# Performance work log

Hardware: AMD Instinct MI355X
Metric: run time of the kernel (lower is better)

The kernel has to match this reference:

```python
import jax, jax.numpy as jnp
import numpy as np


def setup_inputs() -> dict:
    key = jax.random.key(0)
    kq, kk, kv = jax.random.split(key, 3)
    B, N, M, H, D = 4, 2048, 2048, 8, 64
    queries = jax.random.normal(kq, (B, N, H, D), dtype=jnp.float32)
    keys = jax.random.normal(kk, (B, M, H, D), dtype=jnp.float32)
    values = jax.random.normal(kv, (B, M, H, D), dtype=jnp.float32)
    return {"queries": queries, "keys": keys, "values": values}


def reference(queries, keys, values):
    # queries: [B,N,H,D], keys/values: [B,M,H,D]
    D = queries.shape[3]
    softmax_temp = 1.0 / (D ** 0.5)
    QK = jnp.einsum('bnhd,bmhd->bnmh', queries, keys)  # [B,N,M,H]
    A = jax.nn.softmax(softmax_temp * QK, axis=2)      # softmax over M
    queried_values = jnp.einsum('bnmh,bmhd->bnhd', A, values)
    attention_weight = jnp.transpose(A, (0, 3, 1, 2))  # [B,H,N,M]
    return (queried_values, attention_weight)
```

## Files before the change

### kernel.cpp

```cpp
#include <hip/hip_runtime.h>

typedef __bf16 bf16x8 __attribute__((ext_vector_type(8)));
typedef float floatx4 __attribute__((ext_vector_type(4)));
typedef unsigned short ushort8 __attribute__((ext_vector_type(8)));
typedef unsigned short ushort4v __attribute__((ext_vector_type(4)));

#define MFMA(a, b, c) __builtin_amdgcn_mfma_f32_16x16x32_bf16((a), (b), (c), 0, 0, 0)

__device__ __forceinline__ unsigned short f2bf(float x) {
  union { float f; unsigned u; } v; v.f = x;
  unsigned r = v.u + 0x7FFFu + ((v.u >> 16) & 1u);
  return (unsigned short)(r >> 16);
}

constexpr int LD = 72;

__global__ __launch_bounds__(256, 4)
void attn_fwd(const float* __restrict__ Q, const float* __restrict__ K,
              const float* __restrict__ V, float* __restrict__ outQV,
              float* __restrict__ outA)
{
  __shared__ __align__(16) unsigned short Ks[64 * LD];
  __shared__ __align__(16) unsigned short Vts[64 * LD];
  __shared__ __align__(16) unsigned short As[64 * LD];

  const int tid = threadIdx.x;
  const int w  = tid >> 6;
  const int l  = tid & 63;
  const int c  = l & 15;
  const int q4 = l >> 4;

  const int bx = blockIdx.x;
  const int qt = bx & 31;
  const int h  = (bx >> 5) & 7;
  const int b  = bx >> 8;
  const int q0 = qt * 64;

  const float scale = 0.125f * 1.44269504088896340736f;

  const size_t base = (size_t)b * (2048 * 512) + (size_t)h * 64;
  const float* Qb = Q + base + (size_t)q0 * 512;
  const float* Kb = K + base;
  const float* Vb = V + base;

  const int r0 = tid >> 4;
  const int c4 = tid & 15;

  bf16x8 bQ0, bQ1;
  {
    const float* qp = Qb + (size_t)(16 * w + c) * 512 + q4 * 8;
    float4 qa0 = *(const float4*)(qp);
    float4 qa1 = *(const float4*)(qp + 4);
    float4 qb0 = *(const float4*)(qp + 32);
    float4 qb1 = *(const float4*)(qp + 36);
    ushort8 t0, t1;
    t0[0]=f2bf(qa0.x*scale); t0[1]=f2bf(qa0.y*scale); t0[2]=f2bf(qa0.z*scale); t0[3]=f2bf(qa0.w*scale);
    t0[4]=f2bf(qa1.x*scale); t0[5]=f2bf(qa1.y*scale); t0[6]=f2bf(qa1.z*scale); t0[7]=f2bf(qa1.w*scale);
    t1[0]=f2bf(qb0.x*scale); t1[1]=f2bf(qb0.y*scale); t1[2]=f2bf(qb0.z*scale); t1[3]=f2bf(qb0.w*scale);
    t1[4]=f2bf(qb1.x*scale); t1[5]=f2bf(qb1.y*scale); t1[6]=f2bf(qb1.z*scale); t1[7]=f2bf(qb1.w*scale);
    bQ0 = __builtin_bit_cast(bf16x8, t0);
    bQ1 = __builtin_bit_cast(bf16x8, t1);
  }

  float4 kreg[4];
  #pragma unroll
  for (int g = 0; g < 4; ++g)
    kreg[g] = *(const float4*)(Kb + (size_t)(r0 + 16 * g) * 512 + c4 * 4);

  float lsum[4] = {0.f, 0.f, 0.f, 0.f};
  for (int mc = 0; mc < 2048; mc += 64) {
    #pragma unroll
    for (int g = 0; g < 4; ++g) {
      unsigned short* dst = &Ks[(r0 + 16 * g) * LD + c4 * 4];
      dst[0] = f2bf(kreg[g].x); dst[1] = f2bf(kreg[g].y);
      dst[2] = f2bf(kreg[g].z); dst[3] = f2bf(kreg[g].w);
    }
    __syncthreads();
    if (mc + 64 < 2048) {
      #pragma unroll
      for (int g = 0; g < 4; ++g)
        kreg[g] = *(const float4*)(Kb + (size_t)(mc + 64 + r0 + 16 * g) * 512 + c4 * 4);
    }
    #pragma unroll
    for (int t = 0; t < 4; ++t) {
      bf16x8 aK0 = *(const bf16x8*)&Ks[(t * 16 + c) * LD + q4 * 8];
      bf16x8 aK1 = *(const bf16x8*)&Ks[(t * 16 + c) * LD + 32 + q4 * 8];
      floatx4 acc = {0.f, 0.f, 0.f, 0.f};
      acc = MFMA(aK0, bQ0, acc);
      acc = MFMA(aK1, bQ1, acc);
      #pragma unroll
      for (int i = 0; i < 4; ++i) lsum[i] += __builtin_amdgcn_exp2f(acc[i]);
    }
    __syncthreads();
  }
  float rs = (lsum[0] + lsum[1]) + (lsum[2] + lsum[3]);
  rs += __shfl_xor(rs, 16);
  rs += __shfl_xor(rs, 32);
  const float rcp = 1.0f / rs;

  floatx4 Oacc[4];
  #pragma unroll
  for (int t = 0; t < 4; ++t) Oacc[t] = (floatx4){0.f, 0.f, 0.f, 0.f};

  float* aRowP = outA + (((size_t)(b * 8 + h) * 2048 + q0 + 16 * w + c) * 2048) + q4 * 4;

  float4 vreg[4];
  #pragma unroll
  for (int g = 0; g < 4; ++g) {
    kreg[g] = *(const float4*)(Kb + (size_t)(r0 + 16 * g) * 512 + c4 * 4);
    vreg[g] = *(const float4*)(Vb + (size_t)(r0 + 16 * g) * 512 + c4 * 4);
  }

  for (int mc = 0; mc < 2048; mc += 64) {
    #pragma unroll
    for (int g = 0; g < 4; ++g) {
      unsigned short* dst = &Ks[(r0 + 16 * g) * LD + c4 * 4];
      dst[0] = f2bf(kreg[g].x); dst[1] = f2bf(kreg[g].y);
      dst[2] = f2bf(kreg[g].z); dst[3] = f2bf(kreg[g].w);
      int m = r0 + 16 * g;
      Vts[(c4 * 4 + 0) * LD + m] = f2bf(vreg[g].x);
      Vts[(c4 * 4 + 1) * LD + m] = f2bf(vreg[g].y);
      Vts[(c4 * 4 + 2) * LD + m] = f2bf(vreg[g].z);
      Vts[(c4 * 4 + 3) * LD + m] = f2bf(vreg[g].w);
    }
    __syncthreads();
    if (mc + 64 < 2048) {
      #pragma unroll
      for (int g = 0; g < 4; ++g) {
        kreg[g] = *(const float4*)(Kb + (size_t)(mc + 64 + r0 + 16 * g) * 512 + c4 * 4);
        vreg[g] = *(const float4*)(Vb + (size_t)(mc + 64 + r0 + 16 * g) * 512 + c4 * 4);
      }
    }
    #pragma unroll
    for (int t = 0; t < 4; ++t) {
      bf16x8 aK0 = *(const bf16x8*)&Ks[(t * 16 + c) * LD + q4 * 8];
      bf16x8 aK1 = *(const bf16x8*)&Ks[(t * 16 + c) * LD + 32 + q4 * 8];
      floatx4 acc = {0.f, 0.f, 0.f, 0.f};
      acc = MFMA(aK0, bQ0, acc);
      acc = MFMA(aK1, bQ1, acc);
      floatx4 av;
      av[0] = __builtin_amdgcn_exp2f(acc[0]) * rcp;
      av[1] = __builtin_amdgcn_exp2f(acc[1]) * rcp;
      av[2] = __builtin_amdgcn_exp2f(acc[2]) * rcp;
      av[3] = __builtin_amdgcn_exp2f(acc[3]) * rcp;
      __builtin_nontemporal_store(av, (floatx4*)(aRowP + mc + t * 16));
      ushort4v us = { f2bf(av[0]), f2bf(av[1]), f2bf(av[2]), f2bf(av[3]) };
      *(ushort4v*)&As[(16 * w + c) * LD + t * 16 + q4 * 4] = us;
    }
    bf16x8 aP0 = *(const bf16x8*)&As[(16 * w + c) * LD + q4 * 8];
    bf16x8 aP1 = *(const bf16x8*)&As[(16 * w + c) * LD + 32 + q4 * 8];
    #pragma unroll
    for (int t = 0; t < 4; ++t) {
      bf16x8 bV0 = *(const bf16x8*)&Vts[(t * 16 + c) * LD + q4 * 8];
      bf16x8 bV1 = *(const bf16x8*)&Vts[(t * 16 + c) * LD + 32 + q4 * 8];
      Oacc[t] = MFMA(aP0, bV0, Oacc[t]);
      Oacc[t] = MFMA(aP1, bV1, Oacc[t]);
    }
    __syncthreads();
  }

  #pragma unroll
  for (int t = 0; t < 4; ++t) {
    #pragma unroll
    for (int i = 0; i < 4; ++i) {
      outQV[base + (size_t)(q0 + 16 * w + q4 * 4 + i) * 512 + t * 16 + c] = Oacc[t][i];
    }
  }
}

extern "C" void kernel_launch(void* const* d_in, const int* in_sizes, int n_in,
                              void* d_out, int out_size, void* d_ws, size_t ws_size,
                              hipStream_t stream)
{
  const float* Q = (const float*)d_in[0];
  const float* K = (const float*)d_in[1];
  const float* V = (const float*)d_in[2];
  float* outQV = (float*)d_out;
  float* outA  = (float*)d_out + 4194304;
  attn_fwd<<<dim3(1024), dim3(256), 0, stream>>>(Q, K, V, outQV, outA);
}
```

Baseline: 723.0 us.

## Precompute bf16 K and transposed V, stream tiles via direct global-to-LDS double buffering

```diff
diff --git a/kernel.cpp b/kernel.cpp
--- a/kernel.cpp
+++ b/kernel.cpp
@@ -13,16 +13,61 @@
   return (unsigned short)(r >> 16);
 }
 
-constexpr int LD = 72;
+__global__ __launch_bounds__(256)
+void prep(const float* __restrict__ K, const float* __restrict__ V,
+          unsigned short* __restrict__ Kb, unsigned short* __restrict__ Vt)
+{
+  int id = blockIdx.x * 256 + threadIdx.x;
+  int isV = id >> 19;
+  int cch = id & 524287;
+  int bh = cch >> 14;
+  int mt = (cch >> 9) & 31;
+  int g  = cch & 511;
+  int r  = g >> 3;
+  int s  = g & 7;
+  int e8 = s ^ (r & 7);
+  int b = bh >> 3, h = bh & 7;
+  ushort8 o;
+  if (!isV) {
+    const float* p = K + (((size_t)(b * 2048 + mt * 64 + r) * 8 + h) * 64 + e8 * 8);
+    float4 x0 = *(const float4*)p;
+    float4 x1 = *(const float4*)(p + 4);
+    o[0] = f2bf(x0.x); o[1] = f2bf(x0.y); o[2] = f2bf(x0.z); o[3] = f2bf(x0.w);
+    o[4] = f2bf(x1.x); o[5] = f2bf(x1.y); o[6] = f2bf(x1.z); o[7] = f2bf(x1.w);
+    *(ushort8*)(Kb + (size_t)cch * 8) = o;
+  } else {
+    const float* p = V + (((size_t)(b * 2048 + mt * 64 + e8 * 8) * 8 + h) * 64 + r);
+    #pragma unroll
+    for (int j = 0; j < 8; ++j) o[j] = f2bf(p[(size_t)j * 512]);
+    *(ushort8*)(Vt + (size_t)cch * 8) = o;
+  }
+}
+
+__device__ __forceinline__ void stage2k(const unsigned short* gsrc, unsigned short* lds,
+                                        int w, int l)
+{
+  const char* g = (const char*)gsrc + w * 2048 + l * 16;
+  char* sd = (char*)lds + w * 2048;
+  __builtin_amdgcn_global_load_lds((const __attribute__((address_space(1))) unsigned int*)g,
+                                   (__attribute__((address_space(3))) unsigned int*)sd, 16, 0, 0);
+  __builtin_amdgcn_global_load_lds((const __attribute__((address_space(1))) unsigned int*)(g + 1024),
+                                   (__attribute__((address_space(3))) unsigned int*)(sd + 1024), 16, 0, 0);
+}
+
+__device__ __forceinline__ bf16x8 frag(const unsigned short* lds, int r, int bo)
+{
+  int slot = ((bo >> 4) ^ r) & 7;
+  return *(const bf16x8*)((const char*)lds + r * 128 + (slot << 4));
+}
 
 __global__ __launch_bounds__(256, 4)
-void attn_fwd(const float* __restrict__ Q, const float* __restrict__ K,
-              const float* __restrict__ V, float* __restrict__ outQV,
-              float* __restrict__ outA)
-{
-  __shared__ __align__(16) unsigned short Ks[64 * LD];
-  __shared__ __align__(16) unsigned short Vts[64 * LD];
-  __shared__ __align__(16) unsigned short As[64 * LD];
+void attn_fwd(const float* __restrict__ Q, const unsigned short* __restrict__ Kb,
+              const unsigned short* __restrict__ Vt,
+              float* __restrict__ outQV, float* __restrict__ outA)
+{
+  __shared__ __align__(16) unsigned short Ks[2][4096];
+  __shared__ __align__(16) unsigned short Vs[2][4096];
+  __shared__ __align__(16) unsigned short As[4096];
 
   const int tid = threadIdx.x;
   const int w  = tid >> 6;
@@ -40,11 +85,9 @@
 
   const size_t base = (size_t)b * (2048 * 512) + (size_t)h * 64;
   const float* Qb = Q + base + (size_t)q0 * 512;
-  const float* Kb = K + base;
-  const float* Vb = V + base;
-
-  const int r0 = tid >> 4;
-  const int c4 = tid & 15;
+
+  const unsigned short* Kt0 = Kb + (size_t)(b * 8 + h) * (32 * 4096);
+  const unsigned short* Vt0 = Vt + (size_t)(b * 8 + h) * (32 * 4096);
 
   bf16x8 bQ0, bQ1;
   {
@@ -62,36 +105,24 @@
     bQ1 = __builtin_bit_cast(bf16x8, t1);
   }
 
-  float4 kreg[4];
-  #pragma unroll
-  for (int g = 0; g < 4; ++g)
-    kreg[g] = *(const float4*)(Kb + (size_t)(r0 + 16 * g) * 512 + c4 * 4);
-
+  stage2k(Kt0, Ks[0], w, l);
   float lsum[4] = {0.f, 0.f, 0.f, 0.f};
-  for (int mc = 0; mc < 2048; mc += 64) {
-    #pragma unroll
-    for (int g = 0; g < 4; ++g) {
-      unsigned short* dst = &Ks[(r0 + 16 * g) * LD + c4 * 4];
-      dst[0] = f2bf(kreg[g].x); dst[1] = f2bf(kreg[g].y);
-      dst[2] = f2bf(kreg[g].z); dst[3] = f2bf(kreg[g].w);
-    }
+  int cur = 0;
+  for (int mt = 0; mt < 32; ++mt) {
     __syncthreads();
-    if (mc + 64 < 2048) {
-      #pragma unroll
-      for (int g = 0; g < 4; ++g)
-        kreg[g] = *(const float4*)(Kb + (size_t)(mc + 64 + r0 + 16 * g) * 512 + c4 * 4);
-    }
+    if (mt + 1 < 32) stage2k(Kt0 + (size_t)(mt + 1) * 4096, Ks[cur ^ 1], w, l);
+    const unsigned short* Kc = Ks[cur];
     #pragma unroll
     for (int t = 0; t < 4; ++t) {
-      bf16x8 aK0 = *(const bf16x8*)&Ks[(t * 16 + c) * LD + q4 * 8];
-      bf16x8 aK1 = *(const bf16x8*)&Ks[(t * 16 + c) * LD + 32 + q4 * 8];
+      bf16x8 aK0 = frag(Kc, t * 16 + c, q4 * 16);
+      bf16x8 aK1 = frag(Kc, t * 16 + c, 64 + q4 * 16);
       floatx4 acc = {0.f, 0.f, 0.f, 0.f};
       acc = MFMA(aK0, bQ0, acc);
       acc = MFMA(aK1, bQ1, acc);
       #pragma unroll
       for (int i = 0; i < 4; ++i) lsum[i] += __builtin_amdgcn_exp2f(acc[i]);
     }
-    __syncthreads();
+    cur ^= 1;
   }
   float rs = (lsum[0] + lsum[1]) + (lsum[2] + lsum[3]);
   rs += __shfl_xor(rs, 16);
@@ -102,39 +133,26 @@
   #pragma unroll
   for (int t = 0; t < 4; ++t) Oacc[t] = (floatx4){0.f, 0.f, 0.f, 0.f};
 
-  float* aRowP = outA + (((size_t)(b * 8 + h) * 2048 + q0 + 16 * w + c) * 2048) + q4 * 4;
-
-  float4 vreg[4];
-  #pragma unroll
-  for (int g = 0; g < 4; ++g) {
-    kreg[g] = *(const float4*)(Kb + (size_t)(r0 + 16 * g) * 512 + c4 * 4);
-    vreg[g] = *(const float4*)(Vb + (size_t)(r0 + 16 * g) * 512 + c4 * 4);
-  }
-
-  for (int mc = 0; mc < 2048; mc += 64) {
-    #pragma unroll
-    for (int g = 0; g < 4; ++g) {
-      unsigned short* dst = &Ks[(r0 + 16 * g) * LD + c4 * 4];
-      dst[0] = f2bf(kreg[g].x); dst[1] = f2bf(kreg[g].y);
-      dst[2] = f2bf(kreg[g].z); dst[3] = f2bf(kreg[g].w);
-      int m = r0 + 16 * g;
-      Vts[(c4 * 4 + 0) * LD + m] = f2bf(vreg[g].x);
-      Vts[(c4 * 4 + 1) * LD + m] = f2bf(vreg[g].y);
-      Vts[(c4 * 4 + 2) * LD + m] = f2bf(vreg[g].z);
-      Vts[(c4 * 4 + 3) * LD + m] = f2bf(vreg[g].w);
-    }
+  const int arow = 16 * w + c;
+  float* aRowP = outA + (((size_t)(b * 8 + h) * 2048 + q0 + arow) * 2048) + q4 * 4;
+
+  __syncthreads();
+  stage2k(Kt0, Ks[0], w, l);
+  stage2k(Vt0, Vs[0], w, l);
+  cur = 0;
+  for (int mt = 0; mt < 32; ++mt) {
     __syncthreads();
-    if (mc + 64 < 2048) {
-      #pragma unroll
-      for (int g = 0; g < 4; ++g) {
-        kreg[g] = *(const float4*)(Kb + (size_t)(mc + 64 + r0 + 16 * g) * 512 + c4 * 4);
-        vreg[g] = *(const float4*)(Vb + (size_t)(mc + 64 + r0 + 16 * g) * 512 + c4 * 4);
-      }
-    }
+    if (mt + 1 < 32) {
+      stage2k(Kt0 + (size_t)(mt + 1) * 4096, Ks[cur ^ 1], w, l);
+      stage2k(Vt0 + (size_t)(mt + 1) * 4096, Vs[cur ^ 1], w, l);
+    }
+    const unsigned short* Kc = Ks[cur];
+    const unsigned short* Vc = Vs[cur];
+    const int mc = mt * 64;
     #pragma unroll
     for (int t = 0; t < 4; ++t) {
-      bf16x8 aK0 = *(const bf16x8*)&Ks[(t * 16 + c) * LD + q4 * 8];
-      bf16x8 aK1 = *(const bf16x8*)&Ks[(t * 16 + c) * LD + 32 + q4 * 8];
+      bf16x8 aK0 = frag(Kc, t * 16 + c, q4 * 16);
+      bf16x8 aK1 = frag(Kc, t * 16 + c, 64 + q4 * 16);
       floatx4 acc = {0.f, 0.f, 0.f, 0.f};
       acc = MFMA(aK0, bQ0, acc);
       acc = MFMA(aK1, bQ1, acc);
@@ -145,18 +163,20 @@
       av[3] = __builtin_amdgcn_exp2f(acc[3]) * rcp;
       __builtin_nontemporal_store(av, (floatx4*)(aRowP + mc + t * 16));
       ushort4v us = { f2bf(av[0]), f2bf(av[1]), f2bf(av[2]), f2bf(av[3]) };
-      *(ushort4v*)&As[(16 * w + c) * LD + t * 16 + q4 * 4] = us;
-    }
-    bf16x8 aP0 = *(const bf16x8*)&As[(16 * w + c) * LD + q4 * 8];
-    bf16x8 aP1 = *(const bf16x8*)&As[(16 * w + c) * LD + 32 + q4 * 8];
+      int bo = t * 32 + q4 * 8;
+      int slot = ((bo >> 4) ^ arow) & 7;
+      *(ushort4v*)((char*)As + arow * 128 + (slot << 4) + (bo & 15)) = us;
+    }
+    bf16x8 aP0 = frag(As, arow, q4 * 16);
+    bf16x8 aP1 = frag(As, arow, 64 + q4 * 16);
     #pragma unroll
     for (int t = 0; t < 4; ++t) {
-      bf16x8 bV0 = *(const bf16x8*)&Vts[(t * 16 + c) * LD + q4 * 8];
-      bf16x8 bV1 = *(const bf16x8*)&Vts[(t * 16 + c) * LD + 32 + q4 * 8];
+      bf16x8 bV0 = frag(Vc, t * 16 + c, q4 * 16);
+      bf16x8 bV1 = frag(Vc, t * 16 + c, 64 + q4 * 16);
       Oacc[t] = MFMA(aP0, bV0, Oacc[t]);
       Oacc[t] = MFMA(aP1, bV1, Oacc[t]);
     }
-    __syncthreads();
+    cur ^= 1;
   }
 
   #pragma unroll
@@ -177,5 +197,10 @@
   const float* V = (const float*)d_in[2];
   float* outQV = (float*)d_out;
   float* outA  = (float*)d_out + 4194304;
-  attn_fwd<<<dim3(1024), dim3(256), 0, stream>>>(Q, K, V, outQV, outA);
-}
+
+  unsigned short* Kb = (unsigned short*)d_ws;
+  unsigned short* Vt = (unsigned short*)d_ws + 4194304;
+
+  prep<<<dim3(4096), dim3(256), 0, stream>>>(K, V, Kb, Vt);
+  attn_fwd<<<dim3(1024), dim3(256), 0, stream>>>(Q, Kb, Vt, outQV, outA);
+}
```

Measured after the change: 656.2 us. -9.2%, faster.
